# Kernel tuning notes

Measured on AMD Instinct MI355X. Metric: run time of the kernel, lower is better.

Reference implementation:

```python
import jax, jax.numpy as jnp
import numpy as np

KINEMATIC_CHAIN = [[0, 2, 5, 8, 11], [0, 1, 4, 7, 10], [0, 3, 6, 9, 12, 15],
                   [9, 14, 17, 19, 21], [9, 13, 16, 18, 20]]
PATHS = [c[1:] for c in KINEMATIC_CHAIN]  # paths = chain[1:] per gauss_integral_motion
FRAMES, JOINTS = 16384, 22


def setup_inputs() -> dict:
    key = jax.random.key(0)
    k1, k2 = jax.random.split(key)
    motion1 = jax.random.normal(k1, (FRAMES, JOINTS, 3), dtype=jnp.float32)
    motion2 = jax.random.normal(k2, (FRAMES, JOINTS, 3), dtype=jnp.float32)
    return {"motion1": motion1, "motion2": motion2}


def _safe_normalize(v):
    # vec / norm(vec) if norm != 0 else zeros  (matches the torch list comp)
    n = jnp.linalg.norm(v, axis=-1, keepdims=True)
    return jnp.where(n > 0, v / jnp.where(n > 0, n, 1.0), 0.0)


def _gli_pair(p1, p2):
    """Sum of Gauss link integrals over all segment pairs of two paths.
    p1: (L1, 3), p2: (L2, 3) -> scalar. Vectorized over the (L1-1, L2-1) segment grid."""
    s1, e1 = p1[:-1, None, :], p1[1:, None, :]   # (n1, 1, 3)
    s2, e2 = p2[None, :-1, :], p2[None, 1:, :]   # (1, n2, 3)
    r13, r14 = s2 - s1, e2 - s1
    r23, r24 = s2 - e1, e2 - e1
    r12, r34 = e1 - s1, e2 - s2
    faces = [jnp.cross(r13, r14), jnp.cross(r14, r24),
             jnp.cross(r24, r23), jnp.cross(r23, r13)]
    nf = [_safe_normalize(f) for f in faces]
    gli = jnp.zeros(jnp.broadcast_shapes(r13.shape[:-1], r24.shape[:-1]), p1.dtype)
    for i in range(4):
        d = jnp.clip(jnp.sum(nf[i] * nf[(i + 1) % 4], axis=-1), -1.0, 1.0)
        gli = gli + jnp.arcsin(d)
    sign = jnp.sum(jnp.cross(r34, r12) * r13, axis=-1)
    gli = gli * jnp.where(sign > 0, 1.0, -1.0) / (4.0 * jnp.pi)
    return jnp.sum(gli)


def _window_mask(motion1, motion2):
    # xz bounding-box overlap per frame, then dilate each contiguous run by 1
    # frame on each side (start = count-1, end = count+1-1 in the torch code).
    def bbox(m):  # (F, J, 3) -> min/max over joints of x and z
        x, z = m[..., 0], m[..., 2]
        return x.min(1), x.max(1), z.min(1), z.max(1)
    x1n, x1x, z1n, z1x = bbox(motion1)
    x2n, x2x, z2n, z2x = bbox(motion2)
    ov_x = ~((x1x < x2n) | (x2x < x1n))
    ov_z = ~((z1x < z2n) | (z2x < z1n))
    f = ov_x & ov_z  # (F,) bool
    false1 = jnp.zeros((1,), dtype=bool)
    prev = jnp.concatenate([false1, f[:-1]])
    nxt = jnp.concatenate([f[1:], false1])
    return f | prev | nxt


def _gli_motion(motion1, motion2):
    frame = motion1.shape[0]
    n_paths = len(PATHS)
    mask = _window_mask(motion1, motion2).astype(motion1.dtype)  # (F,)
    # GLI_motion[i, a, b]: vmap each path-pair over frames (25 fixed pairs)
    rows = []
    for pa in PATHS:
        p1 = motion1[:, jnp.asarray(pa), :]  # (F, La, 3)
        cols = []
        for pb in PATHS:
            p2 = motion2[:, jnp.asarray(pb), :]  # (F, Lb, 3)
            cols.append(jax.vmap(_gli_pair)(p1, p2))  # (F,)
        rows.append(jnp.stack(cols, axis=-1))  # (F, n_paths)
    gli = jnp.stack(rows, axis=-2)  # (F, n_paths, n_paths)
    gli = gli * mask[:, None, None]  # frames outside windows stay zero
    vel = jnp.abs(gli[1:] - gli[:-1]).reshape(frame - 1, n_paths * n_paths)
    return jnp.max(vel, axis=1)  # (F-1,)


def reference(motion1, motion2):
    return _gli_motion(motion1, motion2)
```

## Files before the change

### kernel.cpp

```cpp
#include <hip/hip_runtime.h>
#include <math.h>

#define NFRAMES 16384
#define NJOINTS 22
#define NPATHS  5
#define NPAIRS  (NPATHS * NPATHS)
#define NSEG    16

__constant__ int c_seg_s[NSEG]  = {2,5,8,  1,4,7,  3,6,9,12,  14,17,19, 13,16,18};
__constant__ int c_seg_e[NSEG]  = {5,8,11, 4,7,10, 6,9,12,15, 17,19,21, 16,18,20};
__constant__ int c_pstart[NPATHS] = {0, 3, 6, 10, 13};
__constant__ int c_plen[NPATHS]   = {3, 3, 4, 3, 3};

struct F3 { float x, y, z; };
__device__ __forceinline__ F3 mk3(float x, float y, float z) { F3 r; r.x=x; r.y=y; r.z=z; return r; }
__device__ __forceinline__ F3 sub3(F3 a, F3 b) { return mk3(a.x-b.x, a.y-b.y, a.z-b.z); }
__device__ __forceinline__ float dot3(F3 a, F3 b) { return a.x*b.x + a.y*b.y + a.z*b.z; }
__device__ __forceinline__ F3 cross3(F3 a, F3 b) {
    return mk3(a.y*b.z - a.z*b.y,
               a.z*b.x - a.x*b.z,
               a.x*b.y - a.y*b.x);
}

__device__ __forceinline__ float fast_asin(float x) {
    float a = fabsf(x);
    float p = fmaf(a, -0.0012624911f,  0.0066700901f);
    p = fmaf(a, p, -0.0170881256f);
    p = fmaf(a, p,  0.0308918810f);
    p = fmaf(a, p, -0.0501743046f);
    p = fmaf(a, p,  0.0889789874f);
    p = fmaf(a, p, -0.2145988016f);
    p = fmaf(a, p,  1.5707963050f);
    float r = 1.5707963268f - __builtin_amdgcn_sqrtf(1.0f - a) * p;
    return copysignf(r, x);
}

__device__ __forceinline__ float asin_term(float d, float ma, float mb) {
    float rs = __builtin_amdgcn_rsqf(ma * mb);
    float x = fminf(1.0f, fmaxf(-1.0f, d * rs));
    float r = fast_asin(x);
    return (ma > 0.0f && mb > 0.0f) ? r : 0.0f;
}

__global__ __launch_bounds__(256) void k_gli(const float* __restrict__ m1,
                                             const float* __restrict__ m2,
                                             float* __restrict__ gli,
                                             int* __restrict__ ov) {
    __shared__ float sA[NJOINTS * 3];
    __shared__ float sB[NJOINTS * 3];
    __shared__ float sT[257];

    int f = blockIdx.x;
    int t = threadIdx.x;
    const float* a = m1 + (size_t)f * NJOINTS * 3;
    const float* b = m2 + (size_t)f * NJOINTS * 3;
    if (t < NJOINTS * 3) { sA[t] = a[t]; sB[t] = b[t]; }
    __syncthreads();

    int i = t >> 4;
    int j = t & 15;
    int s1o = c_seg_s[i] * 3, e1o = c_seg_e[i] * 3;
    int s2o = c_seg_s[j] * 3, e2o = c_seg_e[j] * 3;
    F3 s1 = mk3(sA[s1o], sA[s1o+1], sA[s1o+2]);
    F3 e1 = mk3(sA[e1o], sA[e1o+1], sA[e1o+2]);
    F3 s2 = mk3(sB[s2o], sB[s2o+1], sB[s2o+2]);
    F3 e2 = mk3(sB[e2o], sB[e2o+1], sB[e2o+2]);

    F3 r12 = sub3(e1, s1);
    F3 r13 = sub3(s2, s1);
    F3 r14 = sub3(e2, s1);

    F3 f0 = cross3(r13, r14);
    F3 c1 = cross3(r12, r13);
    F3 c2 = cross3(r12, r14);
    F3 f2 = sub3(sub3(c2, c1), f0);

    float q0 = dot3(f0, f0);
    float q1 = dot3(c2, c2);
    float q2 = dot3(f2, f2);
    float q3 = dot3(c1, c1);

    float g = asin_term( dot3(f0, c2), q0, q1)
            + asin_term( dot3(c2, f2), q1, q2)
            + asin_term(-dot3(f2, c1), q2, q3)
            + asin_term(-dot3(c1, f0), q3, q0);

    float sg = -dot3(c2, r13);
    sT[t] = (sg > 0.0f) ? g : -g;
    if (t == 0) sT[256] = 0.0f;
    __syncthreads();

    if (t < NPAIRS) {
        int pa = (t * 205) >> 10;
        int pb = t - pa * 5;
        int ia0 = c_pstart[pa], na = c_plen[pa];
        int ib0 = c_pstart[pb], nb = c_plen[pb];
        float s = 0.0f;
#pragma unroll
        for (int ka = 0; ka < 4; ka++) {
#pragma unroll
            for (int kb = 0; kb < 4; kb++) {
                int idx = (ka < na && kb < nb) ? ((ia0 + ka) * 16 + (ib0 + kb)) : 256;
                s += sT[idx];
            }
        }
        gli[(size_t)f * NPAIRS + t] = s * 0.07957747154594767f;
    } else if (t == 64) {
        float x1n = sA[0], x1x = sA[0], z1n = sA[2], z1x = sA[2];
        float x2n = sB[0], x2x = sB[0], z2n = sB[2], z2x = sB[2];
#pragma unroll
        for (int jj = 1; jj < NJOINTS; jj++) {
            float ax = sA[jj*3+0], az = sA[jj*3+2];
            x1n = fminf(x1n, ax); x1x = fmaxf(x1x, ax);
            z1n = fminf(z1n, az); z1x = fmaxf(z1x, az);
            float bx = sB[jj*3+0], bz = sB[jj*3+2];
            x2n = fminf(x2n, bx); x2x = fmaxf(x2x, bx);
            z2n = fminf(z2n, bz); z2x = fmaxf(z2x, bz);
        }
        bool ovx = !((x1x < x2n) || (x2x < x1n));
        bool ovz = !((z1x < z2n) || (z2x < z1n));
        ov[f] = (ovx && ovz) ? 1 : 0;
    }
}

__global__ void k_out(const float* __restrict__ gli, const int* __restrict__ ov,
                      float* __restrict__ out) {
    int f = blockIdx.x * blockDim.x + threadIdx.x;
    if (f >= NFRAMES - 1) return;

    int m0 = ov[f];
    if (f > 0) m0 |= ov[f - 1];
    m0 |= ov[f + 1];

    int m1 = ov[f + 1] | ov[f];
    if (f + 2 <= NFRAMES - 1) m1 |= ov[f + 2];

    float ma = m0 ? 1.0f : 0.0f;
    float mb = m1 ? 1.0f : 0.0f;

    const float* g0 = gli + (size_t)f * NPAIRS;
    const float* g1 = g0 + NPAIRS;
    float v = 0.0f;
#pragma unroll
    for (int jj = 0; jj < NPAIRS; jj++) {
        v = fmaxf(v, fabsf(g1[jj] * mb - g0[jj] * ma));
    }
    out[f] = v;
}

extern "C" void kernel_launch(void* const* d_in, const int* in_sizes, int n_in,
                              void* d_out, int out_size, void* d_ws, size_t ws_size,
                              hipStream_t stream) {
    const float* m1 = (const float*)d_in[0];
    const float* m2 = (const float*)d_in[1];
    float* out = (float*)d_out;

    float* gli = (float*)d_ws;
    int* ov = (int*)(gli + (size_t)NFRAMES * NPAIRS);

    k_gli<<<NFRAMES, 256, 0, stream>>>(m1, m2, gli, ov);

    {
        int threads = 256;
        int blocks = (NFRAMES - 1 + threads - 1) / threads;
        k_out<<<blocks, threads, 0, stream>>>(gli, ov, out);
    }
}
```

Measured before the change: 85.57 us.

## Load joints directly from global, shorten asin polynomial, shuffle-reduce bbox, pad gli rows

Removes the shared-memory staging of joint coordinates and its barrier, so each thread loads its segment endpoints straight from global memory using precomputed float offsets. The asin polynomial drops from 8 to 4 coefficients, a lower-accuracy approximation. The serial bounding-box loop in one thread becomes a wavefront butterfly min/max reduction. The gli rows are padded to a stride of 32 so the output kernel can read them with float4 loads. The changes reduce per-block latency but cost precision in the asin and add redundant global loads.

Measured after the change: 87.78 us. 2.6% more time.

```diff
diff --git a/kernel.cpp b/kernel.cpp
--- a/kernel.cpp
+++ b/kernel.cpp
@@ -6,14 +6,21 @@
 #define NPATHS  5
 #define NPAIRS  (NPATHS * NPATHS)
 #define NSEG    16
+#define GSTRIDE 32
 
-__constant__ int c_seg_s[NSEG]  = {2,5,8,  1,4,7,  3,6,9,12,  14,17,19, 13,16,18};
-__constant__ int c_seg_e[NSEG]  = {5,8,11, 4,7,10, 6,9,12,15, 17,19,21, 16,18,20};
+__constant__ int2 c_seg[NSEG] = {
+    {6,15},{15,24},{24,33},
+    {3,12},{12,21},{21,30},
+    {9,18},{18,27},{27,36},{36,45},
+    {42,51},{51,57},{57,63},
+    {39,48},{48,54},{54,60}
+};
 __constant__ int c_pstart[NPATHS] = {0, 3, 6, 10, 13};
 __constant__ int c_plen[NPATHS]   = {3, 3, 4, 3, 3};
 
 struct F3 { float x, y, z; };
 __device__ __forceinline__ F3 mk3(float x, float y, float z) { F3 r; r.x=x; r.y=y; r.z=z; return r; }
+__device__ __forceinline__ F3 ld3(const float* p) { return mk3(p[0], p[1], p[2]); }
 __device__ __forceinline__ F3 sub3(F3 a, F3 b) { return mk3(a.x-b.x, a.y-b.y, a.z-b.z); }
 __device__ __forceinline__ float dot3(F3 a, F3 b) { return a.x*b.x + a.y*b.y + a.z*b.z; }
 __device__ __forceinline__ F3 cross3(F3 a, F3 b) {
@@ -24,13 +31,9 @@
 
 __device__ __forceinline__ float fast_asin(float x) {
     float a = fabsf(x);
-    float p = fmaf(a, -0.0012624911f,  0.0066700901f);
-    p = fmaf(a, p, -0.0170881256f);
-    p = fmaf(a, p,  0.0308918810f);
-    p = fmaf(a, p, -0.0501743046f);
-    p = fmaf(a, p,  0.0889789874f);
-    p = fmaf(a, p, -0.2145988016f);
-    p = fmaf(a, p,  1.5707963050f);
+    float p = fmaf(a, -0.0187293f,  0.0742610f);
+    p = fmaf(a, p, -0.2121144f);
+    p = fmaf(a, p,  1.5707288f);
     float r = 1.5707963268f - __builtin_amdgcn_sqrtf(1.0f - a) * p;
     return copysignf(r, x);
 }
@@ -42,29 +45,36 @@
     return (ma > 0.0f && mb > 0.0f) ? r : 0.0f;
 }
 
+__device__ __forceinline__ float bfly_min(float v) {
+#pragma unroll
+    for (int k = 1; k < 32; k <<= 1) v = fminf(v, __shfl_xor(v, k, 32));
+    return v;
+}
+__device__ __forceinline__ float bfly_max(float v) {
+#pragma unroll
+    for (int k = 1; k < 32; k <<= 1) v = fmaxf(v, __shfl_xor(v, k, 32));
+    return v;
+}
+
 __global__ __launch_bounds__(256) void k_gli(const float* __restrict__ m1,
                                              const float* __restrict__ m2,
                                              float* __restrict__ gli,
                                              int* __restrict__ ov) {
-    __shared__ float sA[NJOINTS * 3];
-    __shared__ float sB[NJOINTS * 3];
     __shared__ float sT[257];
 
     int f = blockIdx.x;
     int t = threadIdx.x;
-    const float* a = m1 + (size_t)f * NJOINTS * 3;
-    const float* b = m2 + (size_t)f * NJOINTS * 3;
-    if (t < NJOINTS * 3) { sA[t] = a[t]; sB[t] = b[t]; }
-    __syncthreads();
+    const float* a = m1 + (size_t)f * (NJOINTS * 3);
+    const float* b = m2 + (size_t)f * (NJOINTS * 3);
 
     int i = t >> 4;
     int j = t & 15;
-    int s1o = c_seg_s[i] * 3, e1o = c_seg_e[i] * 3;
-    int s2o = c_seg_s[j] * 3, e2o = c_seg_e[j] * 3;
-    F3 s1 = mk3(sA[s1o], sA[s1o+1], sA[s1o+2]);
-    F3 e1 = mk3(sA[e1o], sA[e1o+1], sA[e1o+2]);
-    F3 s2 = mk3(sB[s2o], sB[s2o+1], sB[s2o+2]);
-    F3 e2 = mk3(sB[e2o], sB[e2o+1], sB[e2o+2]);
+    int2 o1 = c_seg[i];
+    int2 o2 = c_seg[j];
+    F3 s1 = ld3(a + o1.x);
+    F3 e1 = ld3(a + o1.y);
+    F3 s2 = ld3(b + o2.x);
+    F3 e2 = ld3(b + o2.y);
 
     F3 r12 = sub3(e1, s1);
     F3 r13 = sub3(s2, s1);
@@ -88,6 +98,22 @@
     float sg = -dot3(c2, r13);
     sT[t] = (sg > 0.0f) ? g : -g;
     if (t == 0) sT[256] = 0.0f;
+
+    if (t >= 64 && t < 128) {
+        int jj = t - 64;
+        if (jj > NJOINTS - 1) jj = NJOINTS - 1;
+        float ax = a[jj * 3 + 0], az = a[jj * 3 + 2];
+        float bx = b[jj * 3 + 0], bz = b[jj * 3 + 2];
+        float x1n = bfly_min(ax), x1x = bfly_max(ax);
+        float z1n = bfly_min(az), z1x = bfly_max(az);
+        float x2n = bfly_min(bx), x2x = bfly_max(bx);
+        float z2n = bfly_min(bz), z2x = bfly_max(bz);
+        if (t == 64) {
+            bool ovx = !((x1x < x2n) || (x2x < x1n));
+            bool ovz = !((z1x < z2n) || (z2x < z1n));
+            ov[f] = (ovx && ovz) ? 1 : 0;
+        }
+    }
     __syncthreads();
 
     if (t < NPAIRS) {
@@ -104,22 +130,7 @@
                 s += sT[idx];
             }
         }
-        gli[(size_t)f * NPAIRS + t] = s * 0.07957747154594767f;
-    } else if (t == 64) {
-        float x1n = sA[0], x1x = sA[0], z1n = sA[2], z1x = sA[2];
-        float x2n = sB[0], x2x = sB[0], z2n = sB[2], z2x = sB[2];
-#pragma unroll
-        for (int jj = 1; jj < NJOINTS; jj++) {
-            float ax = sA[jj*3+0], az = sA[jj*3+2];
-            x1n = fminf(x1n, ax); x1x = fmaxf(x1x, ax);
-            z1n = fminf(z1n, az); z1x = fmaxf(z1x, az);
-            float bx = sB[jj*3+0], bz = sB[jj*3+2];
-            x2n = fminf(x2n, bx); x2x = fmaxf(x2x, bx);
-            z2n = fminf(z2n, bz); z2x = fmaxf(z2x, bz);
-        }
-        bool ovx = !((x1x < x2n) || (x2x < x1n));
-        bool ovz = !((z1x < z2n) || (z2x < z1n));
-        ov[f] = (ovx && ovz) ? 1 : 0;
+        gli[(size_t)f * GSTRIDE + t] = s * 0.07957747154594767f;
     }
 }
 
@@ -138,12 +149,22 @@
     float ma = m0 ? 1.0f : 0.0f;
     float mb = m1 ? 1.0f : 0.0f;
 
-    const float* g0 = gli + (size_t)f * NPAIRS;
-    const float* g1 = g0 + NPAIRS;
+    const float4* g0v = (const float4*)(gli + (size_t)f * GSTRIDE);
+    const float4* g1v = (const float4*)(gli + (size_t)(f + 1) * GSTRIDE);
     float v = 0.0f;
 #pragma unroll
-    for (int jj = 0; jj < NPAIRS; jj++) {
-        v = fmaxf(v, fabsf(g1[jj] * mb - g0[jj] * ma));
+    for (int q = 0; q < 6; q++) {
+        float4 u0 = g0v[q];
+        float4 u1 = g1v[q];
+        v = fmaxf(v, fabsf(u1.x * mb - u0.x * ma));
+        v = fmaxf(v, fabsf(u1.y * mb - u0.y * ma));
+        v = fmaxf(v, fabsf(u1.z * mb - u0.z * ma));
+        v = fmaxf(v, fabsf(u1.w * mb - u0.w * ma));
+    }
+    {
+        float u0 = ((const float*)g0v)[24];
+        float u1 = ((const float*)g1v)[24];
+        v = fmaxf(v, fabsf(u1 * mb - u0 * ma));
     }
     out[f] = v;
 }
@@ -156,7 +177,7 @@
     float* out = (float*)d_out;
 
     float* gli = (float*)d_ws;
-    int* ov = (int*)(gli + (size_t)NFRAMES * NPAIRS);
+    int* ov = (int*)(gli + (size_t)NFRAMES * GSTRIDE);
 
     k_gli<<<NFRAMES, 256, 0, stream>>>(m1, m2, gli, ov);
 
```
